# Kernel optimization log

Measured on AMD Instinct MI355X. Metric: run time of the kernel, lower is better.

Reference implementation:

```python
import jax, jax.numpy as jnp
import numpy as np

B, S, D, H, DFF, PDIM = 16, 1024, 256, 8, 1024, 64
N = B * S
E = 262144
DH = D // H
EPS = 1e-5


def _ln(x, w=None, b=None):
    mu = jnp.mean(x, axis=-1, keepdims=True)
    var = jnp.mean((x - mu) ** 2, axis=-1, keepdims=True)
    xn = (x - mu) * jax.lax.rsqrt(var + EPS)
    if w is not None:
        xn = xn * w + b
    return xn


def setup_inputs() -> dict:
    key = jax.random.key(0)
    ks = jax.random.split(key, 24)
    sc = lambda *s: 0.02
    inp = {
        "x": jax.random.normal(ks[0], (B, S, D), jnp.float32),
        "prop_cond": jax.random.normal(ks[1], (B, PDIM), jnp.float32),
        "edge_index": jax.random.randint(ks[2], (2, E), 0, N, jnp.int64),
        # AdaLN 1 & 2
        "ada1_gw": jax.random.normal(ks[3], (D, PDIM)) * 0.02,
        "ada1_gb": jnp.ones((D,), jnp.float32),
        "ada1_bw": jax.random.normal(ks[4], (D, PDIM)) * 0.02,
        "ada1_bb": jnp.zeros((D,), jnp.float32),
        "ada2_gw": jax.random.normal(ks[5], (D, PDIM)) * 0.02,
        "ada2_gb": jnp.ones((D,), jnp.float32),
        "ada2_bw": jax.random.normal(ks[6], (D, PDIM)) * 0.02,
        "ada2_bb": jnp.zeros((D,), jnp.float32),
        # LayerNorms
        "ln1_w": jnp.ones((D,), jnp.float32), "ln1_b": jnp.zeros((D,), jnp.float32),
        "ln2_w": jnp.ones((D,), jnp.float32), "ln2_b": jnp.zeros((D,), jnp.float32),
        "gln_w": jnp.ones((D,), jnp.float32), "gln_b": jnp.zeros((D,), jnp.float32),
        # MHA
        "in_proj_w": jax.random.normal(ks[7], (3 * D, D)) * 0.02,
        "in_proj_b": jnp.zeros((3 * D,), jnp.float32),
        "out_proj_w": jax.random.normal(ks[8], (D, D)) * 0.02,
        "out_proj_b": jnp.zeros((D,), jnp.float32),
        # FFN
        "ffn_w1": jax.random.normal(ks[9], (DFF, D)) * 0.02,
        "ffn_b1": jnp.zeros((DFF,), jnp.float32),
        "ffn_w2": jax.random.normal(ks[10], (D, DFF)) * 0.02,
        "ffn_b2": jnp.zeros((D,), jnp.float32),
        # GATConv (heads=1, concat=False)
        "gat_w": jax.random.normal(ks[11], (D, D)) * 0.02,
        "gat_att_src": jax.random.normal(ks[12], (D,)) * 0.02,
        "gat_att_dst": jax.random.normal(ks[13], (D,)) * 0.02,
        "gat_bias": jnp.zeros((D,), jnp.float32),
    }
    return inp


def _forward(x, prop_cond, edge_index,
             ada1_gw, ada1_gb, ada1_bw, ada1_bb,
             ada2_gw, ada2_gb, ada2_bw, ada2_bb,
             ln1_w, ln1_b, ln2_w, ln2_b, gln_w, gln_b,
             in_proj_w, in_proj_b, out_proj_w, out_proj_b,
             ffn_w1, ffn_b1, ffn_w2, ffn_b2,
             gat_w, gat_att_src, gat_att_dst, gat_bias):
    # ---- AdaLN 1 + attention block ----
    residual = x
    gamma = (prop_cond @ ada1_gw.T + ada1_gb)[:, None, :]  # [B,1,D]
    beta = (prop_cond @ ada1_bw.T + ada1_bb)[:, None, :]
    xa = gamma * _ln(x) + beta
    xn = _ln(xa, ln1_w, ln1_b)
    qkv = xn @ in_proj_w.T + in_proj_b  # [B,S,3D]
    q, k, v = jnp.split(qkv, 3, axis=-1)
    q = q.reshape(B, S, H, DH)
    k = k.reshape(B, S, H, DH)
    v = v.reshape(B, S, H, DH)
    scores = jnp.einsum("bqhd,bkhd->bhqk", q, k) / jnp.sqrt(jnp.float32(DH))
    attn = jax.nn.softmax(scores, axis=-1)
    ao = jnp.einsum("bhqk,bkhd->bqhd", attn, v).reshape(B, S, D)
    ao = ao @ out_proj_w.T + out_proj_b
    x = residual + ao

    # ---- GATConv over flattened nodes (self-loops, leaky_relu 0.2) ----
    nodes = x.reshape(N, D)
    h = nodes @ gat_w.T  # [N,D]
    ar = jnp.arange(N, dtype=edge_index.dtype)
    src = jnp.concatenate([edge_index[0], ar])
    dst = jnp.concatenate([edge_index[1], ar])
    a_src = h @ gat_att_src  # [N]
    a_dst = h @ gat_att_dst
    e = jax.nn.leaky_relu(a_src[src] + a_dst[dst], 0.2)  # [E+N]
    m = jax.ops.segment_max(e, dst, num_segments=N)
    e = jnp.exp(e - m[dst])
    z = jax.ops.segment_sum(e, dst, num_segments=N)
    alpha = e / z[dst]
    agg = jax.ops.segment_sum(alpha[:, None] * h[src], dst, num_segments=N)
    gnn_out = (agg + gat_bias).reshape(B, S, D)
    x = x + gnn_out
    x = _ln(x, gln_w, gln_b)

    # ---- AdaLN 2 + FFN block ----
    residual = x
    gamma = (prop_cond @ ada2_gw.T + ada2_gb)[:, None, :]
    beta = (prop_cond @ ada2_bw.T + ada2_bb)[:, None, :]
    xa = gamma * _ln(x) + beta
    xn = _ln(xa, ln2_w, ln2_b)
    ff = jax.nn.gelu(xn @ ffn_w1.T + ffn_b1, approximate=False) @ ffn_w2.T + ffn_b2
    return residual + ff


def reference(x, prop_cond, edge_index,
              ada1_gw, ada1_gb, ada1_bw, ada1_bb,
              ada2_gw, ada2_gb, ada2_bw, ada2_bb,
              ln1_w, ln1_b, ln2_w, ln2_b, gln_w, gln_b,
              in_proj_w, in_proj_b, out_proj_w, out_proj_b,
              ffn_w1, ffn_b1, ffn_w2, ffn_b2,
              gat_w, gat_att_src, gat_att_dst, gat_bias):
    return _forward(x, prop_cond, edge_index,
                    ada1_gw, ada1_gb, ada1_bw, ada1_bb,
                    ada2_gw, ada2_gb, ada2_bw, ada2_bb,
                    ln1_w, ln1_b, ln2_w, ln2_b, gln_w, gln_b,
                    in_proj_w, in_proj_b, out_proj_w, out_proj_b,
                    ffn_w1, ffn_b1, ffn_w2, ffn_b2,
                    gat_w, gat_att_src, gat_att_dst, gat_bias)
```

## Files before the change

### kernel.cpp

```cpp
#include <hip/hip_runtime.h>
#include <cmath>

#define B_    16
#define S_    1024
#define D_    256
#define H_    8
#define DH_   32
#define DFF_  1024
#define PDIM_ 64
#define N_    (B_ * S_)
#define E_    262144
#define ETOT_ (E_ + N_)
#define EPS_  1e-5f

typedef __attribute__((ext_vector_type(8))) short bf16x8;
typedef __attribute__((ext_vector_type(8))) unsigned short u16x8;
typedef __attribute__((ext_vector_type(4))) float f32x4;

#define QKV_SEC 8388608
#define QKV_LO  4194304
#define H_LO    4194304

__device__ __forceinline__ float wave_sum(float v) {
#pragma unroll
  for (int m = 1; m < 64; m <<= 1) v += __shfl_xor(v, m, 64);
  return v;
}
__device__ __forceinline__ float wave_max(float v) {
#pragma unroll
  for (int m = 1; m < 64; m <<= 1) v = fmaxf(v, __shfl_xor(v, m, 64));
  return v;
}

__device__ __forceinline__ unsigned short f2bf(float f) {
  unsigned int u = __float_as_uint(f);
  unsigned int r = u + 0x7fffu + ((u >> 16) & 1u);
  return (unsigned short)(r >> 16);
}
__device__ __forceinline__ float bf2f(unsigned short s) {
  return __uint_as_float(((unsigned int)s) << 16);
}
__device__ __forceinline__ void split4(float4 v, ushort4& hi, ushort4& lo) {
  unsigned short h;
  h = f2bf(v.x); hi.x = h; lo.x = f2bf(v.x - bf2f(h));
  h = f2bf(v.y); hi.y = h; lo.y = f2bf(v.y - bf2f(h));
  h = f2bf(v.z); hi.z = h; lo.z = f2bf(v.z - bf2f(h));
  h = f2bf(v.w); hi.w = h; lo.w = f2bf(v.w - bf2f(h));
}
__device__ __forceinline__ ushort4 hi4(float4 v) {
  ushort4 h;
  h.x = f2bf(v.x); h.y = f2bf(v.y); h.z = f2bf(v.z); h.w = f2bf(v.w);
  return h;
}

__global__ __launch_bounds__(256) void gamma_beta_kernel(
    const float* __restrict__ pc,
    const float* __restrict__ g1w, const float* __restrict__ g1b,
    const float* __restrict__ b1w, const float* __restrict__ b1b,
    const float* __restrict__ g2w, const float* __restrict__ g2b,
    const float* __restrict__ b2w, const float* __restrict__ b2b,
    float* __restrict__ gamma1, float* __restrict__ beta1,
    float* __restrict__ gamma2, float* __restrict__ beta2) {
  int i = blockIdx.x * 256 + threadIdx.x;
  if (i >= B_ * D_) return;
  int b = i >> 8, d = i & 255;
  const float* p = pc + b * PDIM_;
  float s1 = 0.f, s2 = 0.f, s3 = 0.f, s4 = 0.f;
#pragma unroll 8
  for (int k = 0; k < PDIM_; ++k) {
    float pv = p[k];
    s1 += pv * g1w[d * PDIM_ + k];
    s2 += pv * b1w[d * PDIM_ + k];
    s3 += pv * g2w[d * PDIM_ + k];
    s4 += pv * b2w[d * PDIM_ + k];
  }
  gamma1[i] = s1 + g1b[d];
  beta1[i]  = s2 + b1b[d];
  gamma2[i] = s3 + g2b[d];
  beta2[i]  = s4 + b2b[d];
}

__global__ __launch_bounds__(256) void adaln_kernel(
    const float* __restrict__ x, const float* __restrict__ gamma,
    const float* __restrict__ beta, const float* __restrict__ lnw,
    const float* __restrict__ lnb, float* __restrict__ out) {
  int wid = threadIdx.x >> 6, lane = threadIdx.x & 63;
  int r = blockIdx.x * 4 + wid;
  int b = r >> 10;
  const int c = lane << 2;
  float4 v = *(const float4*)&x[(size_t)r * D_ + c];
  float sum = wave_sum(v.x + v.y + v.z + v.w);
  float mu = sum * (1.f / D_);
  float d0 = v.x - mu, d1 = v.y - mu, d2 = v.z - mu, d3 = v.w - mu;
  float sq = wave_sum(d0 * d0 + d1 * d1 + d2 * d2 + d3 * d3);
  float rs = rsqrtf(sq * (1.f / D_) + EPS_);
  float4 g  = *(const float4*)&gamma[b * D_ + c];
  float4 be = *(const float4*)&beta[b * D_ + c];
  float a0 = g.x * (d0 * rs) + be.x;
  float a1 = g.y * (d1 * rs) + be.y;
  float a2 = g.z * (d2 * rs) + be.z;
  float a3 = g.w * (d3 * rs) + be.w;
  float sum2 = wave_sum(a0 + a1 + a2 + a3);
  float mu2 = sum2 * (1.f / D_);
  float e0 = a0 - mu2, e1 = a1 - mu2, e2 = a2 - mu2, e3 = a3 - mu2;
  float sq2 = wave_sum(e0 * e0 + e1 * e1 + e2 * e2 + e3 * e3);
  float rs2 = rsqrtf(sq2 * (1.f / D_) + EPS_);
  float4 w  = *(const float4*)&lnw[c];
  float4 bb = *(const float4*)&lnb[c];
  float4 o;
  o.x = e0 * rs2 * w.x + bb.x;
  o.y = e1 * rs2 * w.y + bb.y;
  o.z = e2 * rs2 * w.z + bb.z;
  o.w = e3 * rs2 * w.w + bb.w;
  *(float4*)&out[(size_t)r * D_ + c] = o;
}

template <int EPI, int MS>
__global__ __launch_bounds__(256) void gemm_mfma_kernel(
    const float* __restrict__ A, const float* __restrict__ Wt,
    const float* __restrict__ bias, const float* __restrict__ R,
    float* __restrict__ C, int M, int Nc, int K) {
  __shared__ __align__(16) unsigned short Ah[MS * 32][40];
  __shared__ __align__(16) unsigned short Al[MS * 32][40];
  __shared__ __align__(16) unsigned short Bh[128][40];
  const int t = threadIdx.x;
  const int w = t >> 6, l = t & 63;
  const int lr = l & 15, lg = l >> 4;
  const int bm = blockIdx.y * (MS * 32), bn = blockIdx.x * 128;
  constexpr int SA = (MS == 4) ? 1 : 2;
  constexpr int NA = (MS == 4) ? 4 : 2;
  const int sra = t >> SA;
  const int ska = (t & ((1 << SA) - 1)) * (NA * 4);
  const int srb = t >> 1;
  const int skb = (t & 1) * 16;
  const float* Ap = A + (size_t)(bm + sra) * K + ska;
  const float* Bp = Wt + (size_t)(bn + srb) * K + skb;

  f32x4 acc[MS][4];
#pragma unroll
  for (int i = 0; i < MS; ++i)
#pragma unroll
    for (int j = 0; j < 4; ++j) acc[i][j] = (f32x4){0.f, 0.f, 0.f, 0.f};

  float4 ra[NA], rb[4];
#pragma unroll
  for (int c = 0; c < NA; ++c) ra[c] = *(const float4*)(Ap + c * 4);
#pragma unroll
  for (int c = 0; c < 4; ++c) rb[c] = *(const float4*)(Bp + c * 4);

  const int nk = K >> 5;
  for (int kt = 0; kt < nk; ++kt) {
    __syncthreads();
#pragma unroll
    for (int c = 0; c < NA; ++c) {
      ushort4 h4, l4;
      split4(ra[c], h4, l4);
      *(ushort4*)&Ah[sra][ska + c * 4] = h4;
      *(ushort4*)&Al[sra][ska + c * 4] = l4;
    }
#pragma unroll
    for (int c = 0; c < 4; ++c) {
      *(ushort4*)&Bh[srb][skb + c * 4] = hi4(rb[c]);
    }
    if (kt + 1 < nk) {
      Ap += 32;
      Bp += 32;
#pragma unroll
      for (int c = 0; c < NA; ++c) ra[c] = *(const float4*)(Ap + c * 4);
#pragma unroll
      for (int c = 0; c < 4; ++c) rb[c] = *(const float4*)(Bp + c * 4);
    }
    __syncthreads();
    bf16x8 bhj[4];
#pragma unroll
    for (int j = 0; j < 4; ++j) {
      bhj[j] = *(const bf16x8*)&Bh[(w & 1) * 64 + j * 16 + lr][lg * 8];
    }
#pragma unroll
    for (int i = 0; i < MS; ++i) {
      bf16x8 ahi = *(const bf16x8*)&Ah[(w >> 1) * (MS * 16) + i * 16 + lr][lg * 8];
      bf16x8 ali = *(const bf16x8*)&Al[(w >> 1) * (MS * 16) + i * 16 + lr][lg * 8];
#pragma unroll
      for (int j = 0; j < 4; ++j) {
        acc[i][j] = __builtin_amdgcn_mfma_f32_16x16x32_bf16(ahi, bhj[j], acc[i][j], 0, 0, 0);
        acc[i][j] = __builtin_amdgcn_mfma_f32_16x16x32_bf16(ali, bhj[j], acc[i][j], 0, 0, 0);
      }
    }
  }
#pragma unroll
  for (int i = 0; i < MS; ++i) {
    const int m0 = bm + (w >> 1) * (MS * 16) + i * 16 + lg * 4;
#pragma unroll
    for (int j = 0; j < 4; ++j) {
      const int n = bn + (w & 1) * 64 + j * 16 + lr;
      const float bv = bias ? bias[n] : 0.f;
#pragma unroll
      for (int r = 0; r < 4; ++r) {
        const int m = m0 + r;
        float v = acc[i][j][r] + bv;
        if constexpr (EPI == 3) {
          const int sec = n >> 8, f = n & 255, hh = f >> 5, dd = f & 31;
          if (sec == 0) v *= 0.2550332772677823f;
          unsigned short hi = f2bf(v);
          unsigned short lo = f2bf(v - bf2f(hi));
          unsigned short* qs = (unsigned short*)C + (size_t)sec * QKV_SEC;
          const size_t base =
              ((size_t)((m >> 10) * H_ + hh) * S_ + (m & 1023)) * 32 + dd;
          qs[base] = hi;
          qs[base + QKV_LO] = lo;
        } else if constexpr (EPI == 4) {
          unsigned short hi = f2bf(v);
          unsigned short lo = f2bf(v - bf2f(hi));
          unsigned short* hs = (unsigned short*)C;
          const size_t base = (size_t)m * D_ + n;
          hs[base] = hi;
          hs[base + H_LO] = lo;
        } else {
          const size_t idx = (size_t)m * Nc + n;
          if constexpr (EPI == 1) v = 0.5f * v * (1.f + erff(v * 0.7071067811865476f));
          if constexpr (EPI == 2) v += R[idx];
          C[idx] = v;
        }
      }
    }
  }
}

__global__ __launch_bounds__(256) void attn_kernel(
    const unsigned short* __restrict__ qkvs, float* __restrict__ ao) {
  __shared__ __align__(16) unsigned short KhL[64][40];
  __shared__ __align__(16) unsigned short KlL[64][40];
  __shared__ __align__(16) unsigned short VThL[32][72];
  __shared__ __align__(16) unsigned short VTlL[32][72];
  __shared__ __align__(16) unsigned short PhL[4][16][72];
  __shared__ __align__(16) unsigned short PlL[4][16][72];

  const int t = threadIdx.x;
  const int w = t >> 6;
  const int l = t & 63;
  const int lq = l & 15;
  const int g = l >> 4;
  const int qt = blockIdx.x, h = blockIdx.y, b = blockIdx.z;
  const int qbase = qt * 128 + w * 32;
  const size_t panel = (size_t)(b * H_ + h) * S_;

  const unsigned short* Qh_g = qkvs;
  const unsigned short* Ql_g = qkvs + QKV_LO;
  const unsigned short* Kh_g = qkvs + QKV_SEC;
  const unsigned short* Kl_g = qkvs + QKV_SEC + QKV_LO;
  const unsigned short* Vh_g = qkvs + 2 * QKV_SEC;
  const unsigned short* Vl_g = qkvs + 2 * QKV_SEC + QKV_LO;

  bf16x8 qh[2], ql[2];
#pragma unroll
  for (int qs = 0; qs < 2; ++qs) {
    const size_t qi = (panel + qbase + qs * 16 + lq) * 32 + g * 8;
    qh[qs] = *(const bf16x8*)&Qh_g[qi];
    ql[qs] = *(const bf16x8*)&Ql_g[qi];
  }

  f32x4 oacc[2][2];
  float mrun[2], lrun[2];
#pragma unroll
  for (int qs = 0; qs < 2; ++qs) {
    oacc[qs][0] = (f32x4){0.f, 0.f, 0.f, 0.f};
    oacc[qs][1] = (f32x4){0.f, 0.f, 0.f, 0.f};
    mrun[qs] = -1e30f;
    lrun[qs] = 0.f;
  }

  const int key_s = t >> 2;
  const int dg = t & 3;

  for (int kt = 0; kt < 16; ++kt) {
    __syncthreads();
    {
      const size_t kb = (panel + kt * 64 + key_s) * 32 + dg * 8;
      u16x8 khv = *(const u16x8*)&Kh_g[kb];
      u16x8 klv = *(const u16x8*)&Kl_g[kb];
      *(u16x8*)&KhL[key_s][dg * 8] = khv;
      *(u16x8*)&KlL[key_s][dg * 8] = klv;
      u16x8 vhv = *(const u16x8*)&Vh_g[kb];
      u16x8 vlv = *(const u16x8*)&Vl_g[kb];
#pragma unroll
      for (int j = 0; j < 8; ++j) {
        VThL[dg * 8 + j][key_s] = vhv[j];
        VTlL[dg * 8 + j][key_s] = vlv[j];
      }
    }
    __syncthreads();

    bf16x8 kfh[4], kfl[4];
#pragma unroll
    for (int i = 0; i < 4; ++i) {
      kfh[i] = *(const bf16x8*)&KhL[i * 16 + lq][g * 8];
      kfl[i] = *(const bf16x8*)&KlL[i * 16 + lq][g * 8];
    }

#pragma unroll
    for (int qs = 0; qs < 2; ++qs) {
      f32x4 s[4];
#pragma unroll
      for (int i = 0; i < 4; ++i) {
        f32x4 c = (f32x4){0.f, 0.f, 0.f, 0.f};
        c = __builtin_amdgcn_mfma_f32_16x16x32_bf16(kfh[i], qh[qs], c, 0, 0, 0);
        c = __builtin_amdgcn_mfma_f32_16x16x32_bf16(kfh[i], ql[qs], c, 0, 0, 0);
        c = __builtin_amdgcn_mfma_f32_16x16x32_bf16(kfl[i], qh[qs], c, 0, 0, 0);
        s[i] = c;
      }
      float pm = -1e30f;
#pragma unroll
      for (int i = 0; i < 4; ++i)
#pragma unroll
        for (int r = 0; r < 4; ++r) pm = fmaxf(pm, s[i][r]);
      pm = fmaxf(pm, __shfl_xor(pm, 16, 64));
      pm = fmaxf(pm, __shfl_xor(pm, 32, 64));
      float mnew = fmaxf(mrun[qs], pm);
      float rfac = exp2f(mrun[qs] - mnew);
      mrun[qs] = mnew;
      oacc[qs][0] *= rfac;
      oacc[qs][1] *= rfac;
      float lsum = 0.f;
#pragma unroll
      for (int i = 0; i < 4; ++i) {
        ushort4 hv, lv;
        unsigned short hr[4], lr4[4];
#pragma unroll
        for (int r = 0; r < 4; ++r) {
          float p = exp2f(s[i][r] - mnew);
          lsum += p;
          unsigned short ph = f2bf(p);
          hr[r] = ph;
          lr4[r] = f2bf(p - bf2f(ph));
        }
        hv.x = hr[0]; hv.y = hr[1]; hv.z = hr[2]; hv.w = hr[3];
        lv.x = lr4[0]; lv.y = lr4[1]; lv.z = lr4[2]; lv.w = lr4[3];
        *(ushort4*)&PhL[w][lq][i * 16 + g * 4] = hv;
        *(ushort4*)&PlL[w][lq][i * 16 + g * 4] = lv;
      }
      lsum += __shfl_xor(lsum, 16, 64);
      lsum += __shfl_xor(lsum, 32, 64);
      lrun[qs] = lrun[qs] * rfac + lsum;

#pragma unroll
      for (int kh2 = 0; kh2 < 2; ++kh2) {
        bf16x8 pb = *(const bf16x8*)&PhL[w][lq][kh2 * 32 + g * 8];
        bf16x8 pl = *(const bf16x8*)&PlL[w][lq][kh2 * 32 + g * 8];
#pragma unroll
        for (int d = 0; d < 2; ++d) {
          bf16x8 vh = *(const bf16x8*)&VThL[d * 16 + lq][kh2 * 32 + g * 8];
          bf16x8 vl = *(const bf16x8*)&VTlL[d * 16 + lq][kh2 * 32 + g * 8];
          oacc[qs][d] = __builtin_amdgcn_mfma_f32_16x16x32_bf16(vh, pb, oacc[qs][d], 0, 0, 0);
          oacc[qs][d] = __builtin_amdgcn_mfma_f32_16x16x32_bf16(vh, pl, oacc[qs][d], 0, 0, 0);
          oacc[qs][d] = __builtin_amdgcn_mfma_f32_16x16x32_bf16(vl, pb, oacc[qs][d], 0, 0, 0);
        }
      }
    }
  }

#pragma unroll
  for (int qs = 0; qs < 2; ++qs) {
    float inv = 1.f / lrun[qs];
    const size_t orow =
        ((size_t)(b * S_ + qbase + qs * 16 + lq)) * D_ + h * DH_;
#pragma unroll
    for (int d = 0; d < 2; ++d) {
      float4 ov;
      ov.x = oacc[qs][d][0] * inv;
      ov.y = oacc[qs][d][1] * inv;
      ov.z = oacc[qs][d][2] * inv;
      ov.w = oacc[qs][d][3] * inv;
      *(float4*)&ao[orow + d * 16 + g * 4] = ov;
    }
  }
}

__global__ __launch_bounds__(256) void adot_kernel(
    const unsigned short* __restrict__ hs, const float* __restrict__ att_src,
    const float* __restrict__ att_dst, float* __restrict__ a_src,
    float* __restrict__ a_dst) {
  int wid = threadIdx.x >> 6, lane = threadIdx.x & 63;
  int n = blockIdx.x * 4 + wid;
  const int c = lane << 2;
  ushort4 hh = *(const ushort4*)&hs[(size_t)n * D_ + c];
  ushort4 hl = *(const ushort4*)&hs[H_LO + (size_t)n * D_ + c];
  float h0 = bf2f(hh.x) + bf2f(hl.x);
  float h1 = bf2f(hh.y) + bf2f(hl.y);
  float h2 = bf2f(hh.z) + bf2f(hl.z);
  float h3 = bf2f(hh.w) + bf2f(hl.w);
  float4 as = *(const float4*)&att_src[c];
  float4 ad = *(const float4*)&att_dst[c];
  float s = h0 * as.x + h1 * as.y + h2 * as.z + h3 * as.w;
  float d = h0 * ad.x + h1 * ad.y + h2 * ad.z + h3 * ad.w;
  s = wave_sum(s);
  d = wave_sum(d);
  if (lane == 0) { a_src[n] = s; a_dst[n] = d; }
}

__global__ __launch_bounds__(256) void hist_kernel(
    const int* __restrict__ e_dst, int* __restrict__ counts) {
  int i = blockIdx.x * 256 + threadIdx.x;
  if (i >= ETOT_) return;
  int dst = (i < E_) ? e_dst[i] : (i - E_);
  atomicAdd(&counts[dst], 1);
}

__global__ __launch_bounds__(1024) void scan_kernel(
    const int* __restrict__ counts, int* __restrict__ offsets,
    int* __restrict__ cursor) {
  __shared__ int sums[1024];
  const int t = threadIdx.x;
  int local[16];
  int s = 0;
#pragma unroll
  for (int i = 0; i < 16; ++i) { local[i] = s; s += counts[t * 16 + i]; }
  sums[t] = s;
  __syncthreads();
  for (int off = 1; off < 1024; off <<= 1) {
    int v = (t >= off) ? sums[t - off] : 0;
    __syncthreads();
    sums[t] += v;
    __syncthreads();
  }
  int base = (t > 0) ? sums[t - 1] : 0;
#pragma unroll
  for (int i = 0; i < 16; ++i) {
    int o = base + local[i];
    offsets[t * 16 + i] = o;
    cursor[t * 16 + i] = o;
  }
  if (t == 1023) offsets[N_] = sums[1023];
}

__global__ __launch_bounds__(256) void scatter_kernel(
    const int* __restrict__ e_src, const int* __restrict__ e_dst,
    int* __restrict__ cursor, int* __restrict__ csr_src) {
  int i = blockIdx.x * 256 + threadIdx.x;
  if (i >= ETOT_) return;
  int s = (i < E_) ? e_src[i] : (i - E_);
  int d = (i < E_) ? e_dst[i] : (i - E_);
  int slot = atomicAdd(&cursor[d], 1);
  csr_src[slot] = s;
}

__global__ __launch_bounds__(256) void gat_ln_kernel(
    const unsigned short* __restrict__ hs, const float* __restrict__ a_src,
    const float* __restrict__ a_dst, const int* __restrict__ offsets,
    const int* __restrict__ csr_src, const float* __restrict__ gat_bias,
    const float* __restrict__ x1, const float* __restrict__ gln_w,
    const float* __restrict__ gln_b, float* __restrict__ x2) {
  int wid = threadIdx.x >> 6, lane = threadIdx.x & 63;
  int n = blockIdx.x * 4 + wid;
  const int c = lane << 2;
  int beg = offsets[n], end = offsets[n + 1];
  float adn = a_dst[n];
  float m = -1e30f;
  for (int j = beg + lane; j < end; j += 64) {
    float e = a_src[csr_src[j]] + adn;
    e = (e >= 0.f) ? e : 0.2f * e;
    m = fmaxf(m, e);
  }
  m = wave_max(m);
  float z = 0.f;
  float ac0 = 0.f, ac1 = 0.f, ac2 = 0.f, ac3 = 0.f;
  for (int j0 = beg; j0 < end; j0 += 64) {
    int j = j0 + lane;
    float wgt = 0.f;
    int sidx = 0;
    if (j < end) {
      sidx = csr_src[j];
      float e = a_src[sidx] + adn;
      e = (e >= 0.f) ? e : 0.2f * e;
      wgt = __expf(e - m);
    }
    z += wgt;
    int cnt = min(64, end - j0);
    for (int jj = 0; jj < cnt; ++jj) {
      float ww = __shfl(wgt, jj, 64);
      int ss = __shfl(sidx, jj, 64);
      ushort4 hv = *(const ushort4*)&hs[(size_t)ss * D_ + c];
      ac0 += ww * bf2f(hv.x);
      ac1 += ww * bf2f(hv.y);
      ac2 += ww * bf2f(hv.z);
      ac3 += ww * bf2f(hv.w);
    }
  }
  z = wave_sum(z);
  float inv = 1.f / z;
  float4 bv = *(const float4*)&gat_bias[c];
  float4 xv = *(const float4*)&x1[(size_t)n * D_ + c];
  float v0 = ac0 * inv + bv.x + xv.x;
  float v1 = ac1 * inv + bv.y + xv.y;
  float v2 = ac2 * inv + bv.z + xv.z;
  float v3 = ac3 * inv + bv.w + xv.w;
  float sum = wave_sum(v0 + v1 + v2 + v3);
  float mu = sum * (1.f / D_);
  float d0 = v0 - mu, d1 = v1 - mu, d2 = v2 - mu, d3 = v3 - mu;
  float sq = wave_sum(d0 * d0 + d1 * d1 + d2 * d2 + d3 * d3);
  float rs = rsqrtf(sq * (1.f / D_) + EPS_);
  float4 w4 = *(const float4*)&gln_w[c];
  float4 b4 = *(const float4*)&gln_b[c];
  float4 o;
  o.x = d0 * rs * w4.x + b4.x;
  o.y = d1 * rs * w4.y + b4.y;
  o.z = d2 * rs * w4.z + b4.z;
  o.w = d3 * rs * w4.w + b4.w;
  *(float4*)&x2[(size_t)n * D_ + c] = o;
}

extern "C" void kernel_launch(void* const* d_in, const int* in_sizes, int n_in,
                              void* d_out, int out_size, void* d_ws,
                              size_t ws_size, hipStream_t stream) {
  const float* x         = (const float*)d_in[0];
  const float* prop_cond = (const float*)d_in[1];
  const int*   edges     = (const int*)d_in[2];
  const float* a1gw = (const float*)d_in[3];
  const float* a1gb = (const float*)d_in[4];
  const float* a1bw = (const float*)d_in[5];
  const float* a1bb = (const float*)d_in[6];
  const float* a2gw = (const float*)d_in[7];
  const float* a2gb = (const float*)d_in[8];
  const float* a2bw = (const float*)d_in[9];
  const float* a2bb = (const float*)d_in[10];
  const float* ln1w = (const float*)d_in[11];
  const float* ln1b = (const float*)d_in[12];
  const float* ln2w = (const float*)d_in[13];
  const float* ln2b = (const float*)d_in[14];
  const float* glnw = (const float*)d_in[15];
  const float* glnb = (const float*)d_in[16];
  const float* ipw  = (const float*)d_in[17];
  const float* ipb  = (const float*)d_in[18];
  const float* opw  = (const float*)d_in[19];
  const float* opb  = (const float*)d_in[20];
  const float* f1w  = (const float*)d_in[21];
  const float* f1b  = (const float*)d_in[22];
  const float* f2w  = (const float*)d_in[23];
  const float* f2b  = (const float*)d_in[24];
  const float* gatw = (const float*)d_in[25];
  const float* gats = (const float*)d_in[26];
  const float* gatd = (const float*)d_in[27];
  const float* gatb = (const float*)d_in[28];
  float* out = (float*)d_out;

  const int* e_src = edges;
  const int* e_dst = edges + E_;

  float* W = (float*)d_ws;
  const size_t F_BIG = 0;
  const size_t F_XN  = F_BIG + 16777216;
  const size_t F_X1  = F_XN + 4194304;
  const size_t F_H   = F_X1 + 4194304;
  const size_t F_X2  = F_H + 4194304;
  const size_t F_GB  = F_X2 + 4194304;
  const size_t F_AS  = F_GB + 16384;
  const size_t F_AD  = F_AS + N_;
  const size_t F_INT = F_AD + N_;
  float* buf_big = W + F_BIG;
  float* buf_xn  = W + F_XN;
  float* buf_x1  = W + F_X1;
  float* buf_h   = W + F_H;
  float* buf_x2  = W + F_X2;
  float* gamma1  = W + F_GB;
  float* beta1   = gamma1 + 4096;
  float* gamma2  = beta1 + 4096;
  float* beta2   = gamma2 + 4096;
  float* a_src   = W + F_AS;
  float* a_dst   = W + F_AD;
  int* counts  = (int*)(W + F_INT);
  int* offsets = counts + N_;
  int* cursor  = offsets + N_ + 1;
  int* csr_src = cursor + N_;

  hipMemsetAsync(counts, 0, N_ * sizeof(int), stream);

  gamma_beta_kernel<<<16, 256, 0, stream>>>(prop_cond, a1gw, a1gb, a1bw, a1bb,
                                            a2gw, a2gb, a2bw, a2bb, gamma1,
                                            beta1, gamma2, beta2);
  adaln_kernel<<<N_ / 4, 256, 0, stream>>>(x, gamma1, beta1, ln1w, ln1b, buf_xn);
  gemm_mfma_kernel<3, 4><<<dim3(6, 128), 256, 0, stream>>>(
      buf_xn, ipw, ipb, nullptr, buf_big, N_, 768, 256);
  attn_kernel<<<dim3(8, 8, 16), 256, 0, stream>>>(
      (const unsigned short*)buf_big, buf_xn);
  gemm_mfma_kernel<2, 2><<<dim3(2, 256), 256, 0, stream>>>(
      buf_xn, opw, opb, x, buf_x1, N_, 256, 256);
  gemm_mfma_kernel<4, 2><<<dim3(2, 256), 256, 0, stream>>>(
      buf_x1, gatw, nullptr, nullptr, buf_h, N_, 256, 256);
  adot_kernel<<<N_ / 4, 256, 0, stream>>>((const unsigned short*)buf_h, gats,
                                          gatd, a_src, a_dst);
  hist_kernel<<<(ETOT_ + 255) / 256, 256, 0, stream>>>(e_dst, counts);
  scan_kernel<<<1, 1024, 0, stream>>>(counts, offsets, cursor);
  scatter_kernel<<<(ETOT_ + 255) / 256, 256, 0, stream>>>(e_src, e_dst, cursor,
                                                          csr_src);
  gat_ln_kernel<<<N_ / 4, 256, 0, stream>>>((const unsigned short*)buf_h,
                                            a_src, a_dst, offsets, csr_src,
                                            gatb, buf_x1, glnw, glnb, buf_x2);
  adaln_kernel<<<N_ / 4, 256, 0, stream>>>(buf_x2, gamma2, beta2, ln2w, ln2b,
                                           buf_xn);
  gemm_mfma_kernel<1, 4><<<dim3(8, 128), 256, 0, stream>>>(
      buf_xn, f1w, f1b, nullptr, buf_big, N_, DFF_, 256);
  gemm_mfma_kernel<2, 2><<<dim3(2, 256), 256, 0, stream>>>(
      buf_big, f2w, f2b, buf_x2, out, N_, 256, DFF_);
}
```

Baseline: 476.8 us.

## Store V pre-transposed, remap attention blocks per XCD, lazily rescale softmax

The QKV GEMM epilogue now writes V in a transposed [b,h,d,s] layout, so the attention kernel loads V tiles with vector copies instead of a per-element scatter transpose into shared memory. Attention blocks use a 1D grid remapped so that all query tiles of one head panel run on the same XCD, which should improve L2 reuse of K/V. Online softmax skips the running-max update and accumulator rescale unless the new max exceeds the old one by more than 8 in the exp2 domain, saving exp and multiply work. LDS paddings are changed to cut bank conflicts. The lazy rescale lets probabilities reach up to 2^8 before the next rescale, which could affect bf16 hi/lo split precision slightly.

```diff
diff --git a/kernel.cpp b/kernel.cpp
--- a/kernel.cpp
+++ b/kernel.cpp
@@ -204,8 +204,12 @@
           unsigned short hi = f2bf(v);
           unsigned short lo = f2bf(v - bf2f(hi));
           unsigned short* qs = (unsigned short*)C + (size_t)sec * QKV_SEC;
-          const size_t base =
-              ((size_t)((m >> 10) * H_ + hh) * S_ + (m & 1023)) * 32 + dd;
+          size_t base;
+          if (sec == 2) {
+            base = ((size_t)((m >> 10) * H_ + hh) * 32 + dd) * S_ + (m & 1023);
+          } else {
+            base = ((size_t)((m >> 10) * H_ + hh) * S_ + (m & 1023)) * 32 + dd;
+          }
           qs[base] = hi;
           qs[base + QKV_LO] = lo;
         } else if constexpr (EPI == 4) {
@@ -230,19 +234,24 @@
     const unsigned short* __restrict__ qkvs, float* __restrict__ ao) {
   __shared__ __align__(16) unsigned short KhL[64][40];
   __shared__ __align__(16) unsigned short KlL[64][40];
-  __shared__ __align__(16) unsigned short VThL[32][72];
-  __shared__ __align__(16) unsigned short VTlL[32][72];
-  __shared__ __align__(16) unsigned short PhL[4][16][72];
-  __shared__ __align__(16) unsigned short PlL[4][16][72];
+  __shared__ __align__(16) unsigned short VThL[32][66];
+  __shared__ __align__(16) unsigned short VTlL[32][66];
+  __shared__ __align__(16) unsigned short PhL[4][16][74];
+  __shared__ __align__(16) unsigned short PlL[4][16][74];
 
   const int t = threadIdx.x;
   const int w = t >> 6;
   const int l = t & 63;
   const int lq = l & 15;
   const int g = l >> 4;
-  const int qt = blockIdx.x, h = blockIdx.y, b = blockIdx.z;
+  const int bid = blockIdx.x;
+  const int xcd = bid & 7, idx = bid >> 3;
+  const int qt = idx & 7;
+  const int pan = (idx >> 3) * 8 + xcd;
+  const int h = pan & 7, b = pan >> 3;
   const int qbase = qt * 128 + w * 32;
   const size_t panel = (size_t)(b * H_ + h) * S_;
+  const size_t panelT = (size_t)(b * H_ + h) * 32;
 
   const unsigned short* Qh_g = qkvs;
   const unsigned short* Ql_g = qkvs + QKV_LO;
@@ -271,22 +280,18 @@
 
   const int key_s = t >> 2;
   const int dg = t & 3;
+  const int vr = t >> 3;
+  const int vc = (t & 7) * 8;
 
   for (int kt = 0; kt < 16; ++kt) {
     __syncthreads();
     {
       const size_t kb = (panel + kt * 64 + key_s) * 32 + dg * 8;
-      u16x8 khv = *(const u16x8*)&Kh_g[kb];
-      u16x8 klv = *(const u16x8*)&Kl_g[kb];
-      *(u16x8*)&KhL[key_s][dg * 8] = khv;
-      *(u16x8*)&KlL[key_s][dg * 8] = klv;
-      u16x8 vhv = *(const u16x8*)&Vh_g[kb];
-      u16x8 vlv = *(const u16x8*)&Vl_g[kb];
-#pragma unroll
-      for (int j = 0; j < 8; ++j) {
-        VThL[dg * 8 + j][key_s] = vhv[j];
-        VTlL[dg * 8 + j][key_s] = vlv[j];
-      }
+      *(u16x8*)&KhL[key_s][dg * 8] = *(const u16x8*)&Kh_g[kb];
+      *(u16x8*)&KlL[key_s][dg * 8] = *(const u16x8*)&Kl_g[kb];
+      const size_t vb = (panelT + vr) * S_ + kt * 64 + vc;
+      *(u16x8*)&VThL[vr][vc] = *(const u16x8*)&Vh_g[vb];
+      *(u16x8*)&VTlL[vr][vc] = *(const u16x8*)&Vl_g[vb];
     }
     __syncthreads();
 
@@ -315,11 +320,14 @@
         for (int r = 0; r < 4; ++r) pm = fmaxf(pm, s[i][r]);
       pm = fmaxf(pm, __shfl_xor(pm, 16, 64));
       pm = fmaxf(pm, __shfl_xor(pm, 32, 64));
-      float mnew = fmaxf(mrun[qs], pm);
-      float rfac = exp2f(mrun[qs] - mnew);
-      mrun[qs] = mnew;
-      oacc[qs][0] *= rfac;
-      oacc[qs][1] *= rfac;
+      float rfac = 1.f;
+      if (!__all(pm - mrun[qs] <= 8.f)) {
+        float mnew = fmaxf(mrun[qs], pm);
+        rfac = exp2f(mrun[qs] - mnew);
+        mrun[qs] = mnew;
+        oacc[qs][0] *= rfac;
+        oacc[qs][1] *= rfac;
+      }
       float lsum = 0.f;
 #pragma unroll
       for (int i = 0; i < 4; ++i) {
@@ -327,7 +335,7 @@
         unsigned short hr[4], lr4[4];
 #pragma unroll
         for (int r = 0; r < 4; ++r) {
-          float p = exp2f(s[i][r] - mnew);
+          float p = exp2f(s[i][r] - mrun[qs]);
           lsum += p;
           unsigned short ph = f2bf(p);
           hr[r] = ph;
@@ -579,7 +587,7 @@
   adaln_kernel<<<N_ / 4, 256, 0, stream>>>(x, gamma1, beta1, ln1w, ln1b, buf_xn);
   gemm_mfma_kernel<3, 4><<<dim3(6, 128), 256, 0, stream>>>(
       buf_xn, ipw, ipb, nullptr, buf_big, N_, 768, 256);
-  attn_kernel<<<dim3(8, 8, 16), 256, 0, stream>>>(
+  attn_kernel<<<1024, 256, 0, stream>>>(
       (const unsigned short*)buf_big, buf_xn);
   gemm_mfma_kernel<2, 2><<<dim3(2, 256), 256, 0, stream>>>(
       buf_xn, opw, opb, x, buf_x1, N_, 256, 256);
```

Result: no change. 482.4 us (+1.2%).
